# Kernel tuning notes

Hardware: AMD Instinct MI355X
Metric: run time of the kernel (lower is better)

The kernel has to match this reference:

```python
import jax, jax.numpy as jnp
import numpy as np

B, N, L, D = 4, 2048, 12, 128  # batch, nodes, in_len, d_model


def _glorot(key, shape):
    fan_in = shape[0]
    return jax.random.normal(key, shape, dtype=jnp.float32) / jnp.sqrt(jnp.float32(fan_in))


def setup_inputs() -> dict:
    key = jax.random.key(0)
    ks = jax.random.split(key, 12)
    x = jax.random.normal(ks[0], (B, N, L, D), dtype=jnp.float32)
    adj = jax.random.uniform(ks[1], (N, N), dtype=jnp.float32)  # dense weighted adjacency
    # mlp2: Linear(L*D -> D)
    W_mlp2 = _glorot(ks[2], (L * D, D)); b_mlp2 = jnp.zeros((D,), jnp.float32)
    # GNN: three DenseSAGEConv layers (lin_rel on aggregated, lin_root on self)
    Wr1 = _glorot(ks[3], (D, D)); Wo1 = _glorot(ks[4], (D, D)); b1 = jnp.zeros((D,), jnp.float32)
    Wr2 = _glorot(ks[5], (D, D)); Wo2 = _glorot(ks[6], (D, D)); b2 = jnp.zeros((D,), jnp.float32)
    Wr3 = _glorot(ks[7], (D, D)); Wo3 = _glorot(ks[8], (D, D)); b3 = jnp.zeros((D,), jnp.float32)
    # mlp1: Linear(D -> L*D)
    W_mlp1 = _glorot(ks[9], (D, L * D)); b_mlp1 = jnp.zeros((L * D,), jnp.float32)
    return {"x": x, "adj": adj, "W_mlp2": W_mlp2, "b_mlp2": b_mlp2,
            "Wr1": Wr1, "Wo1": Wo1, "b1": b1,
            "Wr2": Wr2, "Wo2": Wo2, "b2": b2,
            "Wr3": Wr3, "Wo3": Wo3, "b3": b3,
            "W_mlp1": W_mlp1, "b_mlp1": b_mlp1}


def reference(x, adj, W_mlp2, b_mlp2, Wr1, Wo1, b1, Wr2, Wo2, b2, Wr3, Wo3, b3, W_mlp1, b_mlp1):
    b_, n_, l_, d_ = x.shape
    xf = x.reshape(b_, n_, l_ * d_)                      # 'b n l d -> b n (l d)'
    h = xf @ W_mlp2 + b_mlp2                             # mlp2: (B,N,D)
    deg = jnp.clip(adj.sum(axis=-1, keepdims=True), 1.0, None)  # (N,1)

    def sage(hin, Wr, Wo, bb):
        # mean neighbor aggregation: (adj @ h) / deg, then rel + root linear
        agg = jnp.einsum('mn,bnd->bmd', adj, hin) / deg
        return agg @ Wr + hin @ Wo + bb

    h = jax.nn.relu(sage(h, Wr1, Wo1, b1))
    h = jax.nn.relu(sage(h, Wr2, Wo2, b2))
    h = sage(h, Wr3, Wo3, b3)                            # gnn1_embed output (B,N,D)
    out = h @ W_mlp1 + b_mlp1                            # mlp1: (B,N,L*D)
    return out
```

## Files before the change

### kernel.cpp

```cpp
#include <hip/hip_runtime.h>

typedef __attribute__((ext_vector_type(8))) short short8;
typedef __attribute__((ext_vector_type(4))) float floatx4;

__device__ inline short to_bf16s(float f) {
    unsigned u = __builtin_bit_cast(unsigned, f);
    unsigned r = u + 0x7FFFu + ((u >> 16) & 1u);
    return (short)(r >> 16);
}

__device__ inline void dma16(const short* g, short* l) {
    __builtin_amdgcn_global_load_lds(
        (const __attribute__((address_space(1))) unsigned int*)(const void*)g,
        (__attribute__((address_space(3))) unsigned int*)(void*)l,
        16, 0, 0);
}

template <typename T> struct Ld8;
template <> struct Ld8<short> {
    static __device__ inline short8 load(const short* p) { return *(const short8*)p; }
};
template <> struct Ld8<float> {
    static __device__ inline short8 load(const float* p) {
        float4 f0 = *(const float4*)p;
        float4 f1 = *(const float4*)(p + 4);
        short8 r;
        r[0] = to_bf16s(f0.x); r[1] = to_bf16s(f0.y);
        r[2] = to_bf16s(f0.z); r[3] = to_bf16s(f0.w);
        r[4] = to_bf16s(f1.x); r[5] = to_bf16s(f1.y);
        r[6] = to_bf16s(f1.z); r[7] = to_bf16s(f1.w);
        return r;
    }
};

struct PrepArgs {
    const float* adj;
    const float* W2; const float* W1;
    const float* Wr0; const float* Wo0;
    const float* Wr1; const float* Wo1;
    const float* Wr2; const float* Wo2;
    short* adjS; short* W2T; short* W1T;
    short* BigB0; short* BigB1; short* BigB2;
};

__global__ __launch_bounds__(256) void prep(PrepArgs p) {
    int bid = blockIdx.x;
    if (bid < 2048) {
        const float* src = p.adj + (size_t)bid * 2048;
        float s = 0.f;
        for (int c = threadIdx.x; c < 2048; c += 256) s += src[c];
        __shared__ float red[256];
        red[threadIdx.x] = s;
        __syncthreads();
        for (int st = 128; st > 0; st >>= 1) {
            if (threadIdx.x < st) red[threadIdx.x] += red[threadIdx.x + st];
            __syncthreads();
        }
        float d = red[0];
        d = d < 1.f ? 1.f : d;
        float inv = 1.f / d;
        short* dst = p.adjS + (size_t)bid * 2048;
        for (int c = threadIdx.x; c < 2048; c += 256) dst[c] = to_bf16s(src[c] * inv);
        return;
    }
    int t = bid - 2048;
    __shared__ short tile[32][33];
    int tx = threadIdx.x & 31, ty0 = threadIdx.x >> 5;
    const float* in; int C_; int bx, by;
    short* outp; int outld, copies, copystride, outofs;
    if (t < 192) {
        bx = (t & 3) * 32; by = (t >> 2) * 32; in = p.W2; C_ = 128;
        outp = p.W2T; outld = 1536; copies = 1; copystride = 0; outofs = 0;
    } else if (t < 384) {
        int u = t - 192; bx = (u % 48) * 32; by = (u / 48) * 32; in = p.W1; C_ = 1536;
        outp = p.W1T; outld = 128; copies = 1; copystride = 0; outofs = 0;
    } else {
        int u = t - 384; int l = u / 32; int v = u % 32;
        const float* Wr[3] = {p.Wr0, p.Wr1, p.Wr2};
        const float* Wo[3] = {p.Wo0, p.Wo1, p.Wo2};
        short* BB[3] = {p.BigB0, p.BigB1, p.BigB2};
        outp = BB[l]; outld = 640; C_ = 128;
        if (v < 16) { in = Wr[l]; bx = (v & 3) * 32; by = (v >> 2) * 32;
                      copies = 4; copystride = 128; outofs = 0; }
        else { v -= 16; in = Wo[l]; bx = (v & 3) * 32; by = (v >> 2) * 32;
               copies = 1; copystride = 0; outofs = 512; }
    }
    for (int i = ty0; i < 32; i += 8)
        tile[i][tx] = to_bf16s(in[(size_t)(by + i) * C_ + bx + tx]);
    __syncthreads();
    for (int i = ty0; i < 32; i += 8) {
        short v = tile[tx][i];
        for (int c = 0; c < copies; ++c)
            outp[(size_t)(bx + i) * outld + (by + tx) + outofs + c * copystride] = v;
    }
}

__global__ __launch_bounds__(256) void transposeHp(const short* __restrict__ big,
                                                   short* __restrict__ HT) {
    __shared__ short tile[32][33];
    int bx = blockIdx.x * 32;
    int by = blockIdx.y * 32;
    int b = blockIdx.z;
    int tx = threadIdx.x & 31, ty0 = threadIdx.x >> 5;
    for (int i = ty0; i < 32; i += 8)
        tile[i][tx] = big[(size_t)((by + i) * 4 + b) * 640 + 512 + bx + tx];
    __syncthreads();
    for (int i = ty0; i < 32; i += 8)
        HT[(size_t)(b * 128 + bx + i) * 2048 + by + tx] = tile[tx][i];
}

#define LDSTR 72
#define TILE_ELEMS (64 * LDSTR)

template <typename TA>
__global__ __launch_bounds__(256) void gemm64(
    const TA* __restrict__ A, int lda,
    const short* __restrict__ B, int ldb, int kTiles,
    const float* __restrict__ bias,
    short* __restrict__ C, int ldc, int colofs, int relu, int rowmap) {
    __shared__ __align__(16) short lds[4 * TILE_ELEMS];

    int tid = threadIdx.x;
    int blockM = blockIdx.x * 64;
    int blockN = blockIdx.y * 64;

    int srow = tid >> 3;
    int scol = (tid & 7) * 8;

    const TA* Abase = A + (size_t)blockM * lda;
    const short* Bbase = B + (size_t)blockN * ldb;

    short8 ra0, ra1, rb0, rb1;
    ra0 = Ld8<TA>::load(Abase + (size_t)srow * lda + scol);
    ra1 = Ld8<TA>::load(Abase + (size_t)(srow + 32) * lda + scol);
    rb0 = Ld8<short>::load(Bbase + (size_t)srow * ldb + scol);
    rb1 = Ld8<short>::load(Bbase + (size_t)(srow + 32) * ldb + scol);

    floatx4 acc[2][2];
    #pragma unroll
    for (int i = 0; i < 2; ++i)
        #pragma unroll
        for (int j = 0; j < 2; ++j)
            #pragma unroll
            for (int r = 0; r < 4; ++r) acc[i][j][r] = 0.f;

    int lane = tid & 63;
    int w = tid >> 6;
    int wr = w >> 1, wc = w & 1;
    int quad = lane >> 4, l15 = lane & 15;

    for (int it = 0; it < kTiles; ++it) {
        short* As = lds + (it & 1) * (2 * TILE_ELEMS);
        short* Bs = As + TILE_ELEMS;
        *(short8*)(As + srow * LDSTR + scol) = ra0;
        *(short8*)(As + (srow + 32) * LDSTR + scol) = ra1;
        *(short8*)(Bs + srow * LDSTR + scol) = rb0;
        *(short8*)(Bs + (srow + 32) * LDSTR + scol) = rb1;
        __syncthreads();
        if (it + 1 < kTiles) {
            int ko = (it + 1) * 64;
            ra0 = Ld8<TA>::load(Abase + (size_t)srow * lda + ko + scol);
            ra1 = Ld8<TA>::load(Abase + (size_t)(srow + 32) * lda + ko + scol);
            rb0 = Ld8<short>::load(Bbase + (size_t)srow * ldb + ko + scol);
            rb1 = Ld8<short>::load(Bbase + (size_t)(srow + 32) * ldb + ko + scol);
        }
        const short* Arow = As + (wr * 32 + l15) * LDSTR;
        const short* Brow = Bs + (wc * 32 + l15) * LDSTR;
        #pragma unroll
        for (int ks = 0; ks < 2; ++ks) {
            int kof = ks * 32 + quad * 8;
            short8 a0 = *(const short8*)(Arow + kof);
            short8 a1 = *(const short8*)(Arow + 16 * LDSTR + kof);
            short8 b0 = *(const short8*)(Brow + kof);
            short8 b1 = *(const short8*)(Brow + 16 * LDSTR + kof);
            acc[0][0] = __builtin_amdgcn_mfma_f32_16x16x32_bf16(a0, b0, acc[0][0], 0, 0, 0);
            acc[0][1] = __builtin_amdgcn_mfma_f32_16x16x32_bf16(a0, b1, acc[0][1], 0, 0, 0);
            acc[1][0] = __builtin_amdgcn_mfma_f32_16x16x32_bf16(a1, b0, acc[1][0], 0, 0, 0);
            acc[1][1] = __builtin_amdgcn_mfma_f32_16x16x32_bf16(a1, b1, acc[1][1], 0, 0, 0);
        }
        __syncthreads();
    }

    #pragma unroll
    for (int ti = 0; ti < 2; ++ti) {
        #pragma unroll
        for (int tj = 0; tj < 2; ++tj) {
            int col = blockN + wc * 32 + tj * 16 + l15;
            float bv = bias ? bias[col] : 0.f;
            int row0 = blockM + wr * 32 + ti * 16 + quad * 4;
            #pragma unroll
            for (int r = 0; r < 4; ++r) {
                int m = row0 + r;
                float x = acc[ti][tj][r] + bv;
                if (relu) x = x > 0.f ? x : 0.f;
                int orow = rowmap ? (((m & 2047) << 2) | (m >> 11)) : m;
                C[(size_t)orow * ldc + col + colofs] = to_bf16s(x);
            }
        }
    }
}

template <int MODE>
__global__ __launch_bounds__(256) void gemm128(
    const short* __restrict__ A, int lda,
    const short* __restrict__ B, int ldb,
    int kChunkIters, const float* __restrict__ bias,
    void* __restrict__ Cv, int ldc) {
    __shared__ __align__(16) short As[128 * 64];
    __shared__ __align__(16) short Bs[128 * 64];

    int tid = threadIdx.x;
    int blockM = blockIdx.x * 128;
    int blockN = blockIdx.y * 128;
    int kz = blockIdx.z * kChunkIters * 64;

    const short* Ab = A + (size_t)(blockM + (tid >> 3)) * lda + kz + (tid & 7) * 8;
    const short* Bb = B + (size_t)(blockN + (tid >> 3)) * ldb + kz + (tid & 7) * 8;
    short* Al = As + tid * 8;
    short* Bl = Bs + tid * 8;

    floatx4 acc[4][4];
    #pragma unroll
    for (int i = 0; i < 4; ++i)
        #pragma unroll
        for (int j = 0; j < 4; ++j)
            #pragma unroll
            for (int r = 0; r < 4; ++r) acc[i][j][r] = 0.f;

    int lane = tid & 63;
    int w = tid >> 6;
    int wr = w >> 1, wc = w & 1;
    int quad = lane >> 4, l15 = lane & 15;

    for (int it = 0; it < kChunkIters; ++it) {
        const short* Ag = Ab + it * 64;
        const short* Bg = Bb + it * 64;
        #pragma unroll
        for (int r = 0; r < 4; ++r) {
            dma16(Ag + (size_t)r * 32 * lda, Al + r * 2048);
            dma16(Bg + (size_t)r * 32 * ldb, Bl + r * 2048);
        }
        __syncthreads();
        const short* Ar = As + (wr * 64 + l15) * 64;
        const short* Br = Bs + (wc * 64 + l15) * 64;
        #pragma unroll
        for (int ks = 0; ks < 2; ++ks) {
            int kof = ks * 32 + quad * 8;
            short8 af[4], bfr[4];
            #pragma unroll
            for (int i = 0; i < 4; ++i) af[i] = *(const short8*)(Ar + i * 16 * 64 + kof);
            #pragma unroll
            for (int j = 0; j < 4; ++j) bfr[j] = *(const short8*)(Br + j * 16 * 64 + kof);
            #pragma unroll
            for (int i = 0; i < 4; ++i)
                #pragma unroll
                for (int j = 0; j < 4; ++j)
                    acc[i][j] = __builtin_amdgcn_mfma_f32_16x16x32_bf16(af[i], bfr[j], acc[i][j], 0, 0, 0);
        }
        __syncthreads();
    }

    if (MODE == 1) {
        short* Cb = (short*)Cv;
        int colofs = blockIdx.z * 128;
        #pragma unroll
        for (int ti = 0; ti < 4; ++ti) {
            #pragma unroll
            for (int tj = 0; tj < 4; ++tj) {
                int j = blockN + wc * 64 + tj * 16 + l15;
                int jhi = j >> 7, jlo = j & 127;
                int row0 = blockM + wr * 64 + ti * 16 + quad * 4;
                #pragma unroll
                for (int r = 0; r < 4; ++r) {
                    int m = row0 + r;
                    Cb[(size_t)(m * 4 + jhi) * ldc + jlo + colofs] = to_bf16s(acc[ti][tj][r]);
                }
            }
        }
    } else {
        float* Cf = (float*)Cv;
        #pragma unroll
        for (int ti = 0; ti < 4; ++ti) {
            #pragma unroll
            for (int tj = 0; tj < 4; ++tj) {
                int col = blockN + wc * 64 + tj * 16 + l15;
                float bv = bias[col];
                int row0 = blockM + wr * 64 + ti * 16 + quad * 4;
                #pragma unroll
                for (int r = 0; r < 4; ++r) {
                    int mp = row0 + r;
                    int orow = ((mp & 3) << 11) | (mp >> 2);
                    Cf[(size_t)orow * ldc + col] = acc[ti][tj][r] + bv;
                }
            }
        }
    }
}

extern "C" void kernel_launch(void* const* d_in, const int* in_sizes, int n_in,
                              void* d_out, int out_size, void* d_ws, size_t ws_size,
                              hipStream_t stream) {
    const float* x      = (const float*)d_in[0];
    const float* adj    = (const float*)d_in[1];
    const float* W_mlp2 = (const float*)d_in[2];
    const float* b_mlp2 = (const float*)d_in[3];
    const float* Wr1    = (const float*)d_in[4];
    const float* Wo1    = (const float*)d_in[5];
    const float* b1     = (const float*)d_in[6];
    const float* Wr2    = (const float*)d_in[7];
    const float* Wo2    = (const float*)d_in[8];
    const float* b2     = (const float*)d_in[9];
    const float* Wr3    = (const float*)d_in[10];
    const float* Wo3    = (const float*)d_in[11];
    const float* b3     = (const float*)d_in[12];
    const float* W_mlp1 = (const float*)d_in[13];
    const float* b_mlp1 = (const float*)d_in[14];
    float* out = (float*)d_out;

    char* ws = (char*)d_ws;
    size_t off = 0;
    auto alloc = [&](size_t bytes) -> char* {
        char* p = ws + off;
        off = (off + bytes + 255) & ~(size_t)255;
        return p;
    };
    short* W2T  = (short*)alloc(128 * 1536 * 2);
    short* W1T  = (short*)alloc(1536 * 128 * 2);
    short* BigB[3];
    for (int l = 0; l < 3; ++l) BigB[l] = (short*)alloc(128 * 640 * 2);
    short* adjS = (short*)alloc((size_t)2048 * 2048 * 2);
    short* big[4];
    for (int l = 0; l < 4; ++l) big[l] = (short*)alloc((size_t)8192 * 640 * 2);
    short* HT = (short*)alloc((size_t)512 * 2048 * 2);

    dim3 blk(256);

    PrepArgs pa{adj, W_mlp2, W_mlp1, Wr1, Wo1, Wr2, Wo2, Wr3, Wo3,
                adjS, W2T, W1T, BigB[0], BigB[1], BigB[2]};
    prep<<<2528, blk, 0, stream>>>(pa);

    gemm64<float><<<dim3(128, 2), blk, 0, stream>>>(
        x, 1536, W2T, 1536, 24, b_mlp2, big[0], 640, 512, 0, 1);

    const float* biases[3] = {b1, b2, b3};
    for (int l = 0; l < 3; ++l) {
        transposeHp<<<dim3(4, 64, 4), blk, 0, stream>>>(big[l], HT);
        gemm128<1><<<dim3(16, 4, 4), blk, 0, stream>>>(
            adjS, 2048, HT, 2048, 8, nullptr, big[l], 640);
        gemm64<short><<<dim3(128, 2), blk, 0, stream>>>(
            big[l], 640, BigB[l], 640, 10, biases[l], big[l + 1], 640, 512,
            (l < 2) ? 1 : 0, 0);
    }

    gemm128<2><<<dim3(64, 12, 1), blk, 0, stream>>>(
        big[3] + 512, 640, W1T, 128, 2, b_mlp1, out, 1536);
}
```

Measured before the change: 248.3 us.

## Fuse prep, mlp2 and per-layer SAGE stages into fewer kernels

Replaces the prep, mlp2 GEMM, per-layer transpose, aggregation GEMM and linear GEMM sequence with one merged setup kernel, three fused per-layer kernels and a final mlp1 kernel. Each fused layer kernel does the adjacency aggregation for a 64-row tile and then applies the stacked Wr/Wo linear step, bias and ReLU from LDS. It also writes both the row-major and transposed activations, so the separate transpose launches go away. Weight transposes now happen inside the GEMMs, which cuts launches and intermediate traffic. The trade-off is that the layer grid is only 128 blocks with no split-K, so the GPU may be under-filled, and the aggregation loop is no longer double-buffered.

```diff
diff --git a/kernel.cpp b/kernel.cpp
--- a/kernel.cpp
+++ b/kernel.cpp
@@ -2,6 +2,8 @@
 
 typedef __attribute__((ext_vector_type(8))) short short8;
 typedef __attribute__((ext_vector_type(4))) float floatx4;
+
+#define MFMA __builtin_amdgcn_mfma_f32_16x16x32_bf16
 
 __device__ inline short to_bf16s(float f) {
     unsigned u = __builtin_bit_cast(unsigned, f);
@@ -9,215 +11,334 @@
     return (short)(r >> 16);
 }
 
+__device__ inline short8 ld8f(const float* p) {
+    float4 f0 = *(const float4*)p, f1 = *(const float4*)(p + 4);
+    short8 r;
+    r[0] = to_bf16s(f0.x); r[1] = to_bf16s(f0.y);
+    r[2] = to_bf16s(f0.z); r[3] = to_bf16s(f0.w);
+    r[4] = to_bf16s(f1.x); r[5] = to_bf16s(f1.y);
+    r[6] = to_bf16s(f1.z); r[7] = to_bf16s(f1.w);
+    return r;
+}
+
 __device__ inline void dma16(const short* g, short* l) {
     __builtin_amdgcn_global_load_lds(
         (const __attribute__((address_space(1))) unsigned int*)(const void*)g,
-        (__attribute__((address_space(3))) unsigned int*)(void*)l,
-        16, 0, 0);
-}
-
-template <typename T> struct Ld8;
-template <> struct Ld8<short> {
-    static __device__ inline short8 load(const short* p) { return *(const short8*)p; }
+        (__attribute__((address_space(3))) unsigned int*)(void*)l, 16, 0, 0);
+}
+
+struct MegaArgs {
+    const float *x, *adj, *W2, *b2;
+    const float *Wr0, *Wo0, *Wr1, *Wo1, *Wr2, *Wo2;
+    short *adjS, *BB0, *BB1, *BB2, *HP0, *HT0;
 };
-template <> struct Ld8<float> {
-    static __device__ inline short8 load(const float* p) {
-        float4 f0 = *(const float4*)p;
-        float4 f1 = *(const float4*)(p + 4);
-        short8 r;
-        r[0] = to_bf16s(f0.x); r[1] = to_bf16s(f0.y);
-        r[2] = to_bf16s(f0.z); r[3] = to_bf16s(f0.w);
-        r[4] = to_bf16s(f1.x); r[5] = to_bf16s(f1.y);
-        r[6] = to_bf16s(f1.z); r[7] = to_bf16s(f1.w);
-        return r;
-    }
-};
-
-struct PrepArgs {
-    const float* adj;
-    const float* W2; const float* W1;
-    const float* Wr0; const float* Wo0;
-    const float* Wr1; const float* Wo1;
-    const float* Wr2; const float* Wo2;
-    short* adjS; short* W2T; short* W1T;
-    short* BigB0; short* BigB1; short* BigB2;
-};
-
-__global__ __launch_bounds__(256) void prep(PrepArgs p) {
+
+__global__ __launch_bounds__(256) void mega(MegaArgs a) {
+    __shared__ __align__(16) short lds[18432];
+    int tid = threadIdx.x;
     int bid = blockIdx.x;
-    if (bid < 2048) {
-        const float* src = p.adj + (size_t)bid * 2048;
-        float s = 0.f;
-        for (int c = threadIdx.x; c < 2048; c += 256) s += src[c];
-        __shared__ float red[256];
-        red[threadIdx.x] = s;
-        __syncthreads();
-        for (int st = 128; st > 0; st >>= 1) {
-            if (threadIdx.x < st) red[threadIdx.x] += red[threadIdx.x + st];
+
+    if (bid < 256) {
+        int mt = bid >> 1, dt = bid & 1;
+        int b = mt >> 5;
+        int n0 = (mt & 31) * 64;
+        int srow = tid >> 3, scol = (tid & 7) * 8;
+        const float* Abase = a.x + (size_t)(mt * 64) * 1536;
+        int kk = tid >> 2, j0 = (tid & 3) * 16;
+        const float* Bbase = a.W2 + (size_t)kk * 128 + dt * 64 + j0;
+
+        short8 ra0 = ld8f(Abase + (size_t)srow * 1536 + scol);
+        short8 ra1 = ld8f(Abase + (size_t)(srow + 32) * 1536 + scol);
+        float4 bw0 = *(const float4*)(Bbase);
+        float4 bw1 = *(const float4*)(Bbase + 4);
+        float4 bw2 = *(const float4*)(Bbase + 8);
+        float4 bw3 = *(const float4*)(Bbase + 12);
+
+        floatx4 acc[2][2];
+        #pragma unroll
+        for (int i = 0; i < 2; ++i)
+            #pragma unroll
+            for (int j = 0; j < 2; ++j)
+                #pragma unroll
+                for (int r = 0; r < 4; ++r) acc[i][j][r] = 0.f;
+
+        int lane = tid & 63, w = tid >> 6, wr = w >> 1, wc = w & 1;
+        int quad = lane >> 4, l15 = lane & 15;
+
+        for (int it = 0; it < 24; ++it) {
+            short* As = lds + (it & 1) * 9216;
+            short* Bs = As + 4608;
+            *(short8*)(As + srow * 72 + scol) = ra0;
+            *(short8*)(As + (srow + 32) * 72 + scol) = ra1;
+            {
+                const float* fw = (const float*)&bw0;
+                #pragma unroll
+                for (int e = 0; e < 4; ++e) Bs[(j0 + e) * 72 + kk] = to_bf16s(fw[e]);
+                fw = (const float*)&bw1;
+                #pragma unroll
+                for (int e = 0; e < 4; ++e) Bs[(j0 + 4 + e) * 72 + kk] = to_bf16s(fw[e]);
+                fw = (const float*)&bw2;
+                #pragma unroll
+                for (int e = 0; e < 4; ++e) Bs[(j0 + 8 + e) * 72 + kk] = to_bf16s(fw[e]);
+                fw = (const float*)&bw3;
+                #pragma unroll
+                for (int e = 0; e < 4; ++e) Bs[(j0 + 12 + e) * 72 + kk] = to_bf16s(fw[e]);
+            }
             __syncthreads();
-        }
-        float d = red[0];
-        d = d < 1.f ? 1.f : d;
-        float inv = 1.f / d;
-        short* dst = p.adjS + (size_t)bid * 2048;
-        for (int c = threadIdx.x; c < 2048; c += 256) dst[c] = to_bf16s(src[c] * inv);
-        return;
-    }
-    int t = bid - 2048;
-    __shared__ short tile[32][33];
-    int tx = threadIdx.x & 31, ty0 = threadIdx.x >> 5;
-    const float* in; int C_; int bx, by;
-    short* outp; int outld, copies, copystride, outofs;
-    if (t < 192) {
-        bx = (t & 3) * 32; by = (t >> 2) * 32; in = p.W2; C_ = 128;
-        outp = p.W2T; outld = 1536; copies = 1; copystride = 0; outofs = 0;
-    } else if (t < 384) {
-        int u = t - 192; bx = (u % 48) * 32; by = (u / 48) * 32; in = p.W1; C_ = 1536;
-        outp = p.W1T; outld = 128; copies = 1; copystride = 0; outofs = 0;
+            if (it + 1 < 24) {
+                int ko = (it + 1) * 64;
+                ra0 = ld8f(Abase + (size_t)srow * 1536 + ko + scol);
+                ra1 = ld8f(Abase + (size_t)(srow + 32) * 1536 + ko + scol);
+                const float* Bp = Bbase + (size_t)ko * 128;
+                bw0 = *(const float4*)(Bp);
+                bw1 = *(const float4*)(Bp + 4);
+                bw2 = *(const float4*)(Bp + 8);
+                bw3 = *(const float4*)(Bp + 12);
+            }
+            const short* Arow = As + (wr * 32 + l15) * 72;
+            const short* Brow = Bs + (wc * 32 + l15) * 72;
+            #pragma unroll
+            for (int ks = 0; ks < 2; ++ks) {
+                int kof = ks * 32 + quad * 8;
+                short8 a0 = *(const short8*)(Arow + kof);
+                short8 a1 = *(const short8*)(Arow + 16 * 72 + kof);
+                short8 b0 = *(const short8*)(Brow + kof);
+                short8 b1 = *(const short8*)(Brow + 16 * 72 + kof);
+                acc[0][0] = MFMA(a0, b0, acc[0][0], 0, 0, 0);
+                acc[0][1] = MFMA(a0, b1, acc[0][1], 0, 0, 0);
+                acc[1][0] = MFMA(a1, b0, acc[1][0], 0, 0, 0);
+                acc[1][1] = MFMA(a1, b1, acc[1][1], 0, 0, 0);
+            }
+            __syncthreads();
+        }
+        #pragma unroll
+        for (int ti = 0; ti < 2; ++ti)
+            #pragma unroll
+            for (int tj = 0; tj < 2; ++tj) {
+                int col = wc * 32 + tj * 16 + l15;
+                float bv = a.b2[dt * 64 + col];
+                int row0 = wr * 32 + ti * 16 + quad * 4;
+                #pragma unroll
+                for (int r = 0; r < 4; ++r)
+                    lds[(row0 + r) * 72 + col] = to_bf16s(acc[ti][tj][r] + bv);
+            }
+        __syncthreads();
+        {
+            int nl = tid >> 2, c0 = (tid & 3) * 16;
+            short8 v0 = *(const short8*)(lds + nl * 72 + c0);
+            short8 v1 = *(const short8*)(lds + nl * 72 + c0 + 8);
+            short* dst = a.HP0 + (size_t)((n0 + nl) * 4 + b) * 128 + dt * 64 + c0;
+            *(short8*)(dst) = v0;
+            *(short8*)(dst + 8) = v1;
+        }
+        {
+            int d = tid >> 2, nh = (tid & 3) * 16;
+            short tmp[16];
+            #pragma unroll
+            for (int i = 0; i < 16; ++i) tmp[i] = lds[(nh + i) * 72 + d];
+            short* dst = a.HT0 + (size_t)(b * 128 + dt * 64 + d) * 2048 + n0 + nh;
+            *(short8*)(dst) = *(const short8*)(tmp);
+            *(short8*)(dst + 8) = *(const short8*)(tmp + 8);
+        }
+    } else if (bid < 512) {
+        float* red = (float*)lds;
+        int base = (bid - 256) * 8;
+        for (int r = 0; r < 8; ++r) {
+            int row = base + r;
+            const float* src = a.adj + (size_t)row * 2048 + tid * 8;
+            float4 f0 = *(const float4*)src;
+            float4 f1 = *(const float4*)(src + 4);
+            float s = f0.x + f0.y + f0.z + f0.w + f1.x + f1.y + f1.z + f1.w;
+            red[tid] = s;
+            __syncthreads();
+            for (int st = 128; st > 0; st >>= 1) {
+                if (tid < st) red[tid] += red[tid + st];
+                __syncthreads();
+            }
+            float dsum = red[0];
+            __syncthreads();
+            dsum = dsum < 1.f ? 1.f : dsum;
+            float inv = 1.f / dsum;
+            short8 o;
+            o[0] = to_bf16s(f0.x * inv); o[1] = to_bf16s(f0.y * inv);
+            o[2] = to_bf16s(f0.z * inv); o[3] = to_bf16s(f0.w * inv);
+            o[4] = to_bf16s(f1.x * inv); o[5] = to_bf16s(f1.y * inv);
+            o[6] = to_bf16s(f1.z * inv); o[7] = to_bf16s(f1.w * inv);
+            *(short8*)(a.adjS + (size_t)row * 2048 + tid * 8) = o;
+        }
     } else {
-        int u = t - 384; int l = u / 32; int v = u % 32;
-        const float* Wr[3] = {p.Wr0, p.Wr1, p.Wr2};
-        const float* Wo[3] = {p.Wo0, p.Wo1, p.Wo2};
-        short* BB[3] = {p.BigB0, p.BigB1, p.BigB2};
-        outp = BB[l]; outld = 640; C_ = 128;
-        if (v < 16) { in = Wr[l]; bx = (v & 3) * 32; by = (v >> 2) * 32;
-                      copies = 4; copystride = 128; outofs = 0; }
-        else { v -= 16; in = Wo[l]; bx = (v & 3) * 32; by = (v >> 2) * 32;
-               copies = 1; copystride = 0; outofs = 512; }
-    }
-    for (int i = ty0; i < 32; i += 8)
-        tile[i][tx] = to_bf16s(in[(size_t)(by + i) * C_ + bx + tx]);
-    __syncthreads();
-    for (int i = ty0; i < 32; i += 8) {
-        short v = tile[tx][i];
-        for (int c = 0; c < copies; ++c)
-            outp[(size_t)(bx + i) * outld + (by + tx) + outofs + c * copystride] = v;
-    }
-}
-
-__global__ __launch_bounds__(256) void transposeHp(const short* __restrict__ big,
-                                                   short* __restrict__ HT) {
-    __shared__ short tile[32][33];
-    int bx = blockIdx.x * 32;
-    int by = blockIdx.y * 32;
-    int b = blockIdx.z;
-    int tx = threadIdx.x & 31, ty0 = threadIdx.x >> 5;
-    for (int i = ty0; i < 32; i += 8)
-        tile[i][tx] = big[(size_t)((by + i) * 4 + b) * 640 + 512 + bx + tx];
-    __syncthreads();
-    for (int i = ty0; i < 32; i += 8)
-        HT[(size_t)(b * 128 + bx + i) * 2048 + by + tx] = tile[tx][i];
-}
-
-#define LDSTR 72
-#define TILE_ELEMS (64 * LDSTR)
-
-template <typename TA>
-__global__ __launch_bounds__(256) void gemm64(
-    const TA* __restrict__ A, int lda,
-    const short* __restrict__ B, int ldb, int kTiles,
-    const float* __restrict__ bias,
-    short* __restrict__ C, int ldc, int colofs, int relu, int rowmap) {
-    __shared__ __align__(16) short lds[4 * TILE_ELEMS];
-
+        int u = bid - 512;
+        int l = u >> 5, v = u & 31;
+        int j0 = (v & 3) * 32, k0 = (v >> 2) * 32;
+        const float* Wr = l == 0 ? a.Wr0 : l == 1 ? a.Wr1 : a.Wr2;
+        const float* Wo = l == 0 ? a.Wo0 : l == 1 ? a.Wo1 : a.Wo2;
+        short* BB = l == 0 ? a.BB0 : l == 1 ? a.BB1 : a.BB2;
+        short(*tile)[33] = (short(*)[33])lds;
+        int tx = tid & 31, ty = tid >> 5;
+        for (int i = ty; i < 32; i += 8) {
+            int k = k0 + i;
+            const float* srow = (k < 128) ? (Wr + (size_t)k * 128)
+                                          : (Wo + (size_t)(k - 128) * 128);
+            tile[i][tx] = to_bf16s(srow[j0 + tx]);
+        }
+        __syncthreads();
+        for (int i = ty; i < 32; i += 8)
+            BB[(size_t)(j0 + i) * 256 + k0 + tx] = tile[tx][i];
+    }
+}
+
+__global__ __launch_bounds__(256) void layer(
+    const short* __restrict__ adjS, const short* __restrict__ HTin,
+    const short* __restrict__ HPin, const short* __restrict__ BB,
+    const float* __restrict__ bias, short* __restrict__ HPout,
+    short* __restrict__ HTout, int relu) {
+    __shared__ __align__(16) short As[64 * 64];
+    __shared__ __align__(16) short Bs[128 * 64];
+    __shared__ __align__(16) short A2[64 * 264];
     int tid = threadIdx.x;
-    int blockM = blockIdx.x * 64;
-    int blockN = blockIdx.y * 64;
-
-    int srow = tid >> 3;
-    int scol = (tid & 7) * 8;
-
-    const TA* Abase = A + (size_t)blockM * lda;
-    const short* Bbase = B + (size_t)blockN * ldb;
-
-    short8 ra0, ra1, rb0, rb1;
-    ra0 = Ld8<TA>::load(Abase + (size_t)srow * lda + scol);
-    ra1 = Ld8<TA>::load(Abase + (size_t)(srow + 32) * lda + scol);
-    rb0 = Ld8<short>::load(Bbase + (size_t)srow * ldb + scol);
-    rb1 = Ld8<short>::load(Bbase + (size_t)(srow + 32) * ldb + scol);
-
-    floatx4 acc[2][2];
+    int mt = blockIdx.x, b = blockIdx.y;
+    int lane = tid & 63, w = tid >> 6, wr = w >> 1, wc = w & 1;
+    int quad = lane >> 4, l15 = lane & 15;
+
+    const short* Ab = adjS + (size_t)(mt * 64 + (tid >> 3)) * 2048 + (tid & 7) * 8;
+    const short* Bb = HTin + (size_t)(b * 128 + (tid >> 3)) * 2048 + (tid & 7) * 8;
+    short* Al = As + tid * 8;
+    short* Bl = Bs + tid * 8;
+
+    floatx4 acc[2][4];
     #pragma unroll
     for (int i = 0; i < 2; ++i)
         #pragma unroll
-        for (int j = 0; j < 2; ++j)
+        for (int j = 0; j < 4; ++j)
             #pragma unroll
             for (int r = 0; r < 4; ++r) acc[i][j][r] = 0.f;
 
-    int lane = tid & 63;
-    int w = tid >> 6;
-    int wr = w >> 1, wc = w & 1;
-    int quad = lane >> 4, l15 = lane & 15;
-
-    for (int it = 0; it < kTiles; ++it) {
-        short* As = lds + (it & 1) * (2 * TILE_ELEMS);
-        short* Bs = As + TILE_ELEMS;
-        *(short8*)(As + srow * LDSTR + scol) = ra0;
-        *(short8*)(As + (srow + 32) * LDSTR + scol) = ra1;
-        *(short8*)(Bs + srow * LDSTR + scol) = rb0;
-        *(short8*)(Bs + (srow + 32) * LDSTR + scol) = rb1;
-        __syncthreads();
-        if (it + 1 < kTiles) {
-            int ko = (it + 1) * 64;
-            ra0 = Ld8<TA>::load(Abase + (size_t)srow * lda + ko + scol);
-            ra1 = Ld8<TA>::load(Abase + (size_t)(srow + 32) * lda + ko + scol);
-            rb0 = Ld8<short>::load(Bbase + (size_t)srow * ldb + ko + scol);
-            rb1 = Ld8<short>::load(Bbase + (size_t)(srow + 32) * ldb + ko + scol);
-        }
-        const short* Arow = As + (wr * 32 + l15) * LDSTR;
-        const short* Brow = Bs + (wc * 32 + l15) * LDSTR;
+    for (int it = 0; it < 32; ++it) {
+        dma16(Ab + it * 64, Al);
+        dma16(Ab + it * 64 + (size_t)32 * 2048, Al + 2048);
+        #pragma unroll
+        for (int r = 0; r < 4; ++r)
+            dma16(Bb + it * 64 + (size_t)(r * 32) * 2048, Bl + r * 2048);
+        __syncthreads();
+        const short* Ar = As + (wr * 32 + l15) * 64;
+        const short* Br = Bs + (wc * 64 + l15) * 64;
         #pragma unroll
         for (int ks = 0; ks < 2; ++ks) {
             int kof = ks * 32 + quad * 8;
-            short8 a0 = *(const short8*)(Arow + kof);
-            short8 a1 = *(const short8*)(Arow + 16 * LDSTR + kof);
-            short8 b0 = *(const short8*)(Brow + kof);
-            short8 b1 = *(const short8*)(Brow + 16 * LDSTR + kof);
-            acc[0][0] = __builtin_amdgcn_mfma_f32_16x16x32_bf16(a0, b0, acc[0][0], 0, 0, 0);
-            acc[0][1] = __builtin_amdgcn_mfma_f32_16x16x32_bf16(a0, b1, acc[0][1], 0, 0, 0);
-            acc[1][0] = __builtin_amdgcn_mfma_f32_16x16x32_bf16(a1, b0, acc[1][0], 0, 0, 0);
-            acc[1][1] = __builtin_amdgcn_mfma_f32_16x16x32_bf16(a1, b1, acc[1][1], 0, 0, 0);
-        }
-        __syncthreads();
-    }
-
-    #pragma unroll
-    for (int ti = 0; ti < 2; ++ti) {
-        #pragma unroll
-        for (int tj = 0; tj < 2; ++tj) {
-            int col = blockN + wc * 32 + tj * 16 + l15;
-            float bv = bias ? bias[col] : 0.f;
-            int row0 = blockM + wr * 32 + ti * 16 + quad * 4;
+            short8 af[2], bf[4];
+            #pragma unroll
+            for (int i = 0; i < 2; ++i) af[i] = *(const short8*)(Ar + i * 16 * 64 + kof);
+            #pragma unroll
+            for (int j = 0; j < 4; ++j) bf[j] = *(const short8*)(Br + j * 16 * 64 + kof);
+            #pragma unroll
+            for (int i = 0; i < 2; ++i)
+                #pragma unroll
+                for (int j = 0; j < 4; ++j)
+                    acc[i][j] = MFMA(af[i], bf[j], acc[i][j], 0, 0, 0);
+        }
+        __syncthreads();
+    }
+
+    #pragma unroll
+    for (int ti = 0; ti < 2; ++ti)
+        #pragma unroll
+        for (int tj = 0; tj < 4; ++tj) {
+            int jc = wc * 64 + tj * 16 + l15;
+            int row0 = wr * 32 + ti * 16 + quad * 4;
+            #pragma unroll
+            for (int r = 0; r < 4; ++r)
+                A2[(row0 + r) * 264 + jc] = to_bf16s(acc[ti][tj][r]);
+        }
+    {
+        int m = tid >> 2, c0 = (tid & 3) * 32;
+        const short* src = HPin + (size_t)((mt * 64 + m) * 4 + b) * 128 + c0;
+        short* dst = A2 + m * 264 + 128 + c0;
+        #pragma unroll
+        for (int q = 0; q < 4; ++q)
+            *(short8*)(dst + q * 8) = *(const short8*)(src + q * 8);
+    }
+    __syncthreads();
+
+    floatx4 acc2[2][4];
+    #pragma unroll
+    for (int i = 0; i < 2; ++i)
+        #pragma unroll
+        for (int j = 0; j < 4; ++j)
+            #pragma unroll
+            for (int r = 0; r < 4; ++r) acc2[i][j][r] = 0.f;
+
+    for (int kc = 0; kc < 4; ++kc) {
+        #pragma unroll
+        for (int r = 0; r < 4; ++r)
+            dma16(BB + (size_t)((tid >> 3) + r * 32) * 256 + kc * 64 + (tid & 7) * 8,
+                  Bl + r * 2048);
+        __syncthreads();
+        const short* A2r = A2 + (wr * 32 + l15) * 264 + kc * 64;
+        const short* Br = Bs + (wc * 64 + l15) * 64;
+        #pragma unroll
+        for (int ks = 0; ks < 2; ++ks) {
+            int kof = ks * 32 + quad * 8;
+            short8 af[2], bf[4];
+            #pragma unroll
+            for (int i = 0; i < 2; ++i) af[i] = *(const short8*)(A2r + i * 16 * 264 + kof);
+            #pragma unroll
+            for (int j = 0; j < 4; ++j) bf[j] = *(const short8*)(Br + j * 16 * 64 + kof);
+            #pragma unroll
+            for (int i = 0; i < 2; ++i)
+                #pragma unroll
+                for (int j = 0; j < 4; ++j)
+                    acc2[i][j] = MFMA(af[i], bf[j], acc2[i][j], 0, 0, 0);
+        }
+        __syncthreads();
+    }
+
+    #pragma unroll
+    for (int ti = 0; ti < 2; ++ti)
+        #pragma unroll
+        for (int tj = 0; tj < 4; ++tj) {
+            int jc = wc * 64 + tj * 16 + l15;
+            float bv = bias[jc];
+            int row0 = wr * 32 + ti * 16 + quad * 4;
             #pragma unroll
             for (int r = 0; r < 4; ++r) {
-                int m = row0 + r;
-                float x = acc[ti][tj][r] + bv;
-                if (relu) x = x > 0.f ? x : 0.f;
-                int orow = rowmap ? (((m & 2047) << 2) | (m >> 11)) : m;
-                C[(size_t)orow * ldc + col + colofs] = to_bf16s(x);
-            }
-        }
-    }
-}
-
-template <int MODE>
-__global__ __launch_bounds__(256) void gemm128(
-    const short* __restrict__ A, int lda,
-    const short* __restrict__ B, int ldb,
-    int kChunkIters, const float* __restrict__ bias,
-    void* __restrict__ Cv, int ldc) {
+                float xv = acc2[ti][tj][r] + bv;
+                if (relu) xv = xv > 0.f ? xv : 0.f;
+                A2[(row0 + r) * 136 + jc] = to_bf16s(xv);
+            }
+        }
+    __syncthreads();
+    {
+        int m = tid >> 2, c0 = (tid & 3) * 32;
+        const short* src = A2 + m * 136 + c0;
+        short* dst = HPout + (size_t)((mt * 64 + m) * 4 + b) * 128 + c0;
+        #pragma unroll
+        for (int q = 0; q < 4; ++q)
+            *(short8*)(dst + q * 8) = *(const short8*)(src + q * 8);
+    }
+    if (HTout) {
+        int d = tid >> 1, nh = (tid & 1) * 32;
+        short tmp[32];
+        #pragma unroll
+        for (int i = 0; i < 32; ++i) tmp[i] = A2[(nh + i) * 136 + d];
+        short* dst = HTout + (size_t)(b * 128 + d) * 2048 + mt * 64 + nh;
+        #pragma unroll
+        for (int q = 0; q < 4; ++q)
+            *(short8*)(dst + q * 8) = *(const short8*)(tmp + q * 8);
+    }
+}
+
+__global__ __launch_bounds__(256) void mlp1k(
+    const short* __restrict__ HP3, const float* __restrict__ W1,
+    const float* __restrict__ bias, float* __restrict__ out) {
     __shared__ __align__(16) short As[128 * 64];
     __shared__ __align__(16) short Bs[128 * 64];
-
     int tid = threadIdx.x;
     int blockM = blockIdx.x * 128;
     int blockN = blockIdx.y * 128;
-    int kz = blockIdx.z * kChunkIters * 64;
-
-    const short* Ab = A + (size_t)(blockM + (tid >> 3)) * lda + kz + (tid & 7) * 8;
-    const short* Bb = B + (size_t)(blockN + (tid >> 3)) * ldb + kz + (tid & 7) * 8;
+    const short* Ab = HP3 + (size_t)(blockM + (tid >> 3)) * 128 + (tid & 7) * 8;
     short* Al = As + tid * 8;
-    short* Bl = Bs + tid * 8;
+    int kk = tid & 63, c0 = (tid >> 6) * 32;
+    const float* Wb = W1 + (size_t)kk * 1536 + blockN + c0;
 
     floatx4 acc[4][4];
     #pragma unroll
@@ -227,18 +348,23 @@
             #pragma unroll
             for (int r = 0; r < 4; ++r) acc[i][j][r] = 0.f;
 
-    int lane = tid & 63;
-    int w = tid >> 6;
-    int wr = w >> 1, wc = w & 1;
+    int lane = tid & 63, w = tid >> 6, wr = w >> 1, wc = w & 1;
     int quad = lane >> 4, l15 = lane & 15;
 
-    for (int it = 0; it < kChunkIters; ++it) {
-        const short* Ag = Ab + it * 64;
-        const short* Bg = Bb + it * 64;
-        #pragma unroll
-        for (int r = 0; r < 4; ++r) {
-            dma16(Ag + (size_t)r * 32 * lda, Al + r * 2048);
-            dma16(Bg + (size_t)r * 32 * ldb, Bl + r * 2048);
+    for (int it = 0; it < 2; ++it) {
+        #pragma unroll
+        for (int r = 0; r < 4; ++r)
+            dma16(Ab + it * 64 + (size_t)(r * 32) * 128, Al + r * 2048);
+        const float* Wp = Wb + (size_t)it * 64 * 1536;
+        float4 f[8];
+        #pragma unroll
+        for (int q = 0; q < 8; ++q) f[q] = *(const float4*)(Wp + q * 4);
+        #pragma unroll
+        for (int q = 0; q < 8; ++q) {
+            const float* fe = (const float*)&f[q];
+            #pragma unroll
+            for (int e = 0; e < 4; ++e)
+                Bs[(c0 + q * 4 + e) * 64 + kk] = to_bf16s(fe[e]);
         }
         __syncthreads();
         const short* Ar = As + (wr * 64 + l15) * 64;
@@ -246,55 +372,34 @@
         #pragma unroll
         for (int ks = 0; ks < 2; ++ks) {
             int kof = ks * 32 + quad * 8;
-            short8 af[4], bfr[4];
+            short8 af[4], bf[4];
             #pragma unroll
             for (int i = 0; i < 4; ++i) af[i] = *(const short8*)(Ar + i * 16 * 64 + kof);
             #pragma unroll
-            for (int j = 0; j < 4; ++j) bfr[j] = *(const short8*)(Br + j * 16 * 64 + kof);
+            for (int j = 0; j < 4; ++j) bf[j] = *(const short8*)(Br + j * 16 * 64 + kof);
             #pragma unroll
             for (int i = 0; i < 4; ++i)
                 #pragma unroll
                 for (int j = 0; j < 4; ++j)
-                    acc[i][j] = __builtin_amdgcn_mfma_f32_16x16x32_bf16(af[i], bfr[j], acc[i][j], 0, 0, 0);
-        }
-        __syncthreads();
-    }
-
-    if (MODE == 1) {
-        short* Cb = (short*)Cv;
-        int colofs = blockIdx.z * 128;
-        #pragma unroll
-        for (int ti = 0; ti < 4; ++ti) {
-            #pragma unroll
-            for (int tj = 0; tj < 4; ++tj) {
-                int j = blockN + wc * 64 + tj * 16 + l15;
-                int jhi = j >> 7, jlo = j & 127;
-                int row0 = blockM + wr * 64 + ti * 16 + quad * 4;
-                #pragma unroll
-                for (int r = 0; r < 4; ++r) {
-                    int m = row0 + r;
-                    Cb[(size_t)(m * 4 + jhi) * ldc + jlo + colofs] = to_bf16s(acc[ti][tj][r]);
-                }
-            }
-        }
-    } else {
-        float* Cf = (float*)Cv;
-        #pragma unroll
-        for (int ti = 0; ti < 4; ++ti) {
-            #pragma unroll
-            for (int tj = 0; tj < 4; ++tj) {
-                int col = blockN + wc * 64 + tj * 16 + l15;
-                float bv = bias[col];
-                int row0 = blockM + wr * 64 + ti * 16 + quad * 4;
-                #pragma unroll
-                for (int r = 0; r < 4; ++r) {
-                    int mp = row0 + r;
-                    int orow = ((mp & 3) << 11) | (mp >> 2);
-                    Cf[(size_t)orow * ldc + col] = acc[ti][tj][r] + bv;
-                }
-            }
-        }
-    }
+                    acc[i][j] = MFMA(af[i], bf[j], acc[i][j], 0, 0, 0);
+        }
+        __syncthreads();
+    }
+
+    #pragma unroll
+    for (int ti = 0; ti < 4; ++ti)
+        #pragma unroll
+        for (int tj = 0; tj < 4; ++tj) {
+            int col = blockN + wc * 64 + tj * 16 + l15;
+            float bv = bias[col];
+            int row0 = blockM + wr * 64 + ti * 16 + quad * 4;
+            #pragma unroll
+            for (int r = 0; r < 4; ++r) {
+                int mp = row0 + r;
+                int orow = ((mp & 3) << 11) | (mp >> 2);
+                out[(size_t)orow * 1536 + col] = acc[ti][tj][r] + bv;
+            }
+        }
 }
 
 extern "C" void kernel_launch(void* const* d_in, const int* in_sizes, int n_in,
@@ -324,34 +429,19 @@
         off = (off + bytes + 255) & ~(size_t)255;
         return p;
     };
-    short* W2T  = (short*)alloc(128 * 1536 * 2);
-    short* W1T  = (short*)alloc(1536 * 128 * 2);
-    short* BigB[3];
-    for (int l = 0; l < 3; ++l) BigB[l] = (short*)alloc(128 * 640 * 2);
     short* adjS = (short*)alloc((size_t)2048 * 2048 * 2);
-    short* big[4];
-    for (int l = 0; l < 4; ++l) big[l] = (short*)alloc((size_t)8192 * 640 * 2);
-    short* HT = (short*)alloc((size_t)512 * 2048 * 2);
-
-    dim3 blk(256);
-
-    PrepArgs pa{adj, W_mlp2, W_mlp1, Wr1, Wo1, Wr2, Wo2, Wr3, Wo3,
-                adjS, W2T, W1T, BigB[0], BigB[1], BigB[2]};
-    prep<<<2528, blk, 0, stream>>>(pa);
-
-    gemm64<float><<<dim3(128, 2), blk, 0, stream>>>(
-        x, 1536, W2T, 1536, 24, b_mlp2, big[0], 640, 512, 0, 1);
-
-    const float* biases[3] = {b1, b2, b3};
-    for (int l = 0; l < 3; ++l) {
-        transposeHp<<<dim3(4, 64, 4), blk, 0, stream>>>(big[l], HT);
-        gemm128<1><<<dim3(16, 4, 4), blk, 0, stream>>>(
-            adjS, 2048, HT, 2048, 8, nullptr, big[l], 640);
-        gemm64<short><<<dim3(128, 2), blk, 0, stream>>>(
-            big[l], 640, BigB[l], 640, 10, biases[l], big[l + 1], 640, 512,
-            (l < 2) ? 1 : 0, 0);
-    }
-
-    gemm128<2><<<dim3(64, 12, 1), blk, 0, stream>>>(
-        big[3] + 512, 640, W1T, 128, 2, b_mlp1, out, 1536);
-}
+    short* BB[3];
+    for (int l = 0; l < 3; ++l) BB[l] = (short*)alloc(128 * 256 * 2);
+    short* HPa = (short*)alloc((size_t)8192 * 128 * 2);
+    short* HPb = (short*)alloc((size_t)8192 * 128 * 2);
+    short* HTa = (short*)alloc((size_t)512 * 2048 * 2);
+    short* HTb = (short*)alloc((size_t)512 * 2048 * 2);
+
+    MegaArgs ma{x, adj, W_mlp2, b_mlp2, Wr1, Wo1, Wr2, Wo2, Wr3, Wo3,
+                adjS, BB[0], BB[1], BB[2], HPa, HTa};
+    mega<<<608, 256, 0, stream>>>(ma);
+    layer<<<dim3(32, 4), 256, 0, stream>>>(adjS, HTa, HPa, BB[0], b1, HPb, HTb, 1);
+    layer<<<dim3(32, 4), 256, 0, stream>>>(adjS, HTb, HPb, BB[1], b2, HPa, HTa, 1);
+    layer<<<dim3(32, 4), 256, 0, stream>>>(adjS, HTa, HPa, BB[2], b3, HPb, nullptr, 0);
+    mlp1k<<<dim3(64, 12), 256, 0, stream>>>(HPb, W_mlp1, b_mlp1, out);
+}
```

Result: slower. 274.7 us (+10.6%).
